# Kernel tuning notes

Measured on AMD Instinct MI355X. Metric: run time of the kernel, lower is better.

The kernel has to match this reference:

```python
import jax, jax.numpy as jnp
import numpy as np

HEADS = 8
DIM_HEAD = 64
EPS = 1e-5  # PyTorch InstanceNorm default eps


def _instance_norm_lastdim(t):
    # PyTorch InstanceNorm1d on (b*h, n, d) with affine=False normalizes over
    # the last (spatial) axis d per (sample, token), biased variance.
    mu = jnp.mean(t, axis=-1, keepdims=True)
    var = jnp.mean(jnp.square(t - mu), axis=-1, keepdims=True)
    return (t - mu) / jnp.sqrt(var + EPS)


def setup_inputs() -> dict:
    key = jax.random.key(0)
    k1, k2, k3, k4, k5 = jax.random.split(key, 5)
    b, n1, n2, dim = 4, 8192, 8192, 256
    inner = HEADS * DIM_HEAD  # 512
    return {
        "x": jax.random.normal(k1, (b, n1, dim), jnp.float32),
        "z": jax.random.normal(k2, (b, n2, dim), jnp.float32),
        "Wq": jax.random.normal(k3, (dim, inner), jnp.float32) * 0.02,
        "Wkv": jax.random.normal(k4, (dim, 2 * inner), jnp.float32) * 0.02,
        "Wout": jax.random.normal(k5, (inner, dim), jnp.float32) * 0.02,
        "bout": jnp.zeros((dim,), jnp.float32),
    }


def reference(x, z, Wq, Wkv, Wout, bout):
    b, n1, _ = x.shape
    n2 = z.shape[1]
    h, d = HEADS, DIM_HEAD

    q = x @ Wq                     # [b, n1, h*d]
    kv = z @ Wkv                   # [b, n2, 2*h*d]
    k, v = jnp.split(kv, 2, axis=-1)

    q = q.reshape(b, n1, h, d).transpose(0, 2, 1, 3)  # b h n1 d
    k = k.reshape(b, n2, h, d).transpose(0, 2, 1, 3)  # b h n2 d
    v = v.reshape(b, n2, h, d).transpose(0, 2, 1, 3)  # b h n2 d

    # galerkin: normalize k and v
    k = _instance_norm_lastdim(k)
    v = _instance_norm_lastdim(v)

    # linear-attention kernel trick: (k^T v) then q @ dots, scaled by 1/n2
    dots = jnp.einsum('bhnd,bhne->bhde', k, v)          # [b, h, d, d]
    out = jnp.einsum('bhnd,bhde->bhne', q, dots) / n2   # [b, h, n1, d]

    out = out.transpose(0, 2, 1, 3).reshape(b, n1, h * d)
    return out @ Wout + bout
```

## Files before the change

kernel.cpp:

```cpp
#include <hip/hip_runtime.h>
#include <cstddef>

#define NB    4
#define NTOK  8192
#define DIMX  256
#define NH    8
#define HD    64
#define INNER 512
#define SPLIT 32
#define EPS   1e-5f

typedef __attribute__((ext_vector_type(8))) short short8;
typedef __attribute__((ext_vector_type(4))) float f32x4;

__device__ __forceinline__ unsigned short f2bf(float f) {
  union { float f; unsigned u; } v; v.f = f;
  unsigned r = v.u + 0x7fffu + ((v.u >> 16) & 1u);
  return (unsigned short)(r >> 16);
}

__global__ __launch_bounds__(256) void k_pre(
    const float* __restrict__ z, unsigned short* __restrict__ zb,
    const float* __restrict__ Wkv, unsigned short* __restrict__ wkvT)
{
  __shared__ unsigned short t[64][68];
  if (blockIdx.x < 2048) {
    const size_t i = ((size_t)blockIdx.x * 256 + threadIdx.x) * 16;
    float4 a0 = *(const float4*)(z + i);
    float4 a1 = *(const float4*)(z + i + 4);
    float4 a2 = *(const float4*)(z + i + 8);
    float4 a3 = *(const float4*)(z + i + 12);
    short8 p0, p1;
    p0[0] = (short)f2bf(a0.x); p0[1] = (short)f2bf(a0.y);
    p0[2] = (short)f2bf(a0.z); p0[3] = (short)f2bf(a0.w);
    p0[4] = (short)f2bf(a1.x); p0[5] = (short)f2bf(a1.y);
    p0[6] = (short)f2bf(a1.z); p0[7] = (short)f2bf(a1.w);
    p1[0] = (short)f2bf(a2.x); p1[1] = (short)f2bf(a2.y);
    p1[2] = (short)f2bf(a2.z); p1[3] = (short)f2bf(a2.w);
    p1[4] = (short)f2bf(a3.x); p1[5] = (short)f2bf(a3.y);
    p1[6] = (short)f2bf(a3.z); p1[7] = (short)f2bf(a3.w);
    *(short8*)(zb + i) = p0;
    *(short8*)(zb + i + 8) = p1;
  } else {
    const int tid = threadIdx.x;
    const int bb = blockIdx.x - 2048;
    const int r0 = (bb & 3) * 64;
    const int c0 = (bb >> 2) * 64;
    const int r = tid >> 2;
    const int c4 = (tid & 3) * 16;
#pragma unroll
    for (int j = 0; j < 4; ++j) {
      float4 v = *(const float4*)(Wkv + (size_t)(r0 + r) * (2 * INNER) + c0 + c4 + j * 4);
      t[r][c4 + j * 4 + 0] = f2bf(v.x);
      t[r][c4 + j * 4 + 1] = f2bf(v.y);
      t[r][c4 + j * 4 + 2] = f2bf(v.z);
      t[r][c4 + j * 4 + 3] = f2bf(v.w);
    }
    __syncthreads();
    const int cc = tid >> 2;
    const int rr4 = (tid & 3) * 16;
    short8 o0, o1;
#pragma unroll
    for (int i = 0; i < 8; ++i) o0[i] = (short)t[rr4 + i][cc];
#pragma unroll
    for (int i = 0; i < 8; ++i) o1[i] = (short)t[rr4 + 8 + i][cc];
    unsigned short* dst = wkvT + (size_t)(c0 + cc) * DIMX + r0 + rr4;
    *(short8*)(dst) = o0;
    *(short8*)(dst + 8) = o1;
  }
}

__global__ __launch_bounds__(256, 2) void k_dots_mfma(
    const unsigned short* __restrict__ zb, const unsigned short* __restrict__ wkvT,
    float* __restrict__ partial)
{
  const int tid  = threadIdx.x;
  const int lane = tid & 63;
  const int w    = tid >> 6;
  const int wm   = w >> 1;
  const int wn   = w & 1;
  const int l15  = lane & 15;
  const int lg   = lane >> 4;

  const int bid = blockIdx.x;
  const int s = bid & (SPLIT - 1);
  const int h = (bid >> 5) & (NH - 1);
  const int b = bid >> 8;

  __shared__ unsigned short zs[2][32][268];
  __shared__ unsigned short kv2[2][128][36];

  short8 awf[4][8];
#pragma unroll
  for (int mf = 0; mf < 4; ++mf) {
    const int dim = wm * 64 + mf * 16 + l15;
    const int gd = (dim < HD) ? (h * HD + dim) : (INNER + h * HD + (dim - HD));
    const unsigned short* base = wkvT + (size_t)gd * DIMX + lg * 8;
#pragma unroll
    for (int kk = 0; kk < 8; ++kk)
      awf[mf][kk] = *(const short8*)(base + kk * 32);
  }

  f32x4 dacc[4];
#pragma unroll
  for (int nf = 0; nf < 4; ++nf) dacc[nf] = (f32x4){0.f, 0.f, 0.f, 0.f};

  const int zr = tid >> 3;
  const int zc = (tid & 7) * 32;
  const unsigned short* zbase = zb + ((size_t)b * NTOK + s * 256 + zr) * DIMX + zc;

  {
    short8 pre[4];
#pragma unroll
    for (int j = 0; j < 4; ++j) pre[j] = *(const short8*)(zbase + j * 8);
#pragma unroll
    for (int j = 0; j < 4; ++j) *(short8*)&zs[0][zr][zc + j * 8] = pre[j];
  }
  __syncthreads();

  int cur = 0;
  for (int tile = 0; tile < 8; ++tile) {
    short8 pre[4];
    if (tile < 7) {
      const unsigned short* src = zbase + (size_t)(tile + 1) * 32 * DIMX;
#pragma unroll
      for (int j = 0; j < 4; ++j) pre[j] = *(const short8*)(src + j * 8);
    }

    f32x4 acc[4];
#pragma unroll
    for (int mf = 0; mf < 4; ++mf) acc[mf] = (f32x4){0.f, 0.f, 0.f, 0.f};

#pragma unroll
    for (int kk = 0; kk < 8; ++kk) {
      short8 bfr = *(const short8*)&zs[cur][wn * 16 + l15][kk * 32 + lg * 8];
#pragma unroll
      for (int mf = 0; mf < 4; ++mf)
        acc[mf] = __builtin_amdgcn_mfma_f32_16x16x32_bf16(
            awf[mf][kk], bfr, acc[mf], 0, 0, 0);
    }

    float a = 0.f, q = 0.f;
#pragma unroll
    for (int mf = 0; mf < 4; ++mf)
#pragma unroll
      for (int r = 0; r < 4; ++r) {
        float v = acc[mf][r];
        a += v; q += v * v;
      }
    a += __shfl_xor(a, 16); a += __shfl_xor(a, 32);
    q += __shfl_xor(q, 16); q += __shfl_xor(q, 32);
    const float mu = a * (1.f / 64.f);
    const float rs = rsqrtf(q * (1.f / 64.f) - mu * mu + EPS);

#pragma unroll
    for (int mf = 0; mf < 4; ++mf)
#pragma unroll
      for (int r = 0; r < 4; ++r)
        kv2[cur][wm * 64 + mf * 16 + lg * 4 + r][wn * 16 + l15] =
            f2bf((acc[mf][r] - mu) * rs);

    if (tile < 7) {
#pragma unroll
      for (int j = 0; j < 4; ++j) *(short8*)&zs[cur ^ 1][zr][zc + j * 8] = pre[j];
    }
    __syncthreads();

    {
      short8 a2 = *(const short8*)&kv2[cur][w * 16 + l15][lg * 8];
#pragma unroll
      for (int nf = 0; nf < 4; ++nf) {
        short8 b2 = *(const short8*)&kv2[cur][64 + nf * 16 + l15][lg * 8];
        dacc[nf] = __builtin_amdgcn_mfma_f32_16x16x32_bf16(a2, b2, dacc[nf], 0, 0, 0);
      }
    }
    cur ^= 1;
  }

  float* pb = partial + ((size_t)((b * NH + h) * SPLIT + s)) * 4096;
#pragma unroll
  for (int nf = 0; nf < 4; ++nf)
#pragma unroll
    for (int r = 0; r < 4; ++r)
      pb[(w * 16 + lg * 4 + r) * 64 + nf * 16 + l15] = dacc[nf][r];
}

__global__ __launch_bounds__(256) void k_reduce(
    const float* __restrict__ partial, float* __restrict__ dots)
{
  const int idx = blockIdx.x * 256 + threadIdx.x;
  const int bh = idx >> 12;
  const int de = idx & 4095;
  const float* p = partial + (size_t)bh * SPLIT * 4096 + de;
  float s = 0.f;
#pragma unroll
  for (int i = 0; i < SPLIT; ++i) s += p[(size_t)i * 4096];
  dots[idx] = s * (1.f / (float)NTOK);
}

__global__ __launch_bounds__(256) void k_bdwout(
    const float* __restrict__ dots, const float* __restrict__ Wout,
    float* __restrict__ tmp)
{
  const int bid = blockIdx.x;
  const int b = bid >> 7;
  const int r4 = (bid & 127) * 4;
  const int h = r4 >> 6;
  const int c = threadIdx.x;
  const float* dr = dots + (size_t)(b * NH + h) * 4096 + (size_t)(r4 & 63) * 64;
  float a0 = 0.f, a1 = 0.f, a2 = 0.f, a3 = 0.f;
#pragma unroll 8
  for (int j = 0; j < 64; ++j) {
    const float wv = Wout[(size_t)(h * 64 + j) * DIMX + c];
    a0 += dr[j] * wv;
    a1 += dr[64 + j] * wv;
    a2 += dr[128 + j] * wv;
    a3 += dr[192 + j] * wv;
  }
  float* tb = tmp + ((size_t)b * INNER + r4) * DIMX + c;
  tb[0] = a0; tb[DIMX] = a1; tb[2 * DIMX] = a2; tb[3 * DIMX] = a3;
}

__global__ __launch_bounds__(256) void k_weff(
    const float* __restrict__ Wq, const float* __restrict__ tmp,
    unsigned short* __restrict__ weffT)
{
  const int bid = blockIdx.x;
  const int b = bid >> 6;
  const int r4 = (bid & 63) * 4;
  const int c = threadIdx.x;
  const float* tb = tmp + (size_t)b * INNER * DIMX + c;
  float a0 = 0.f, a1 = 0.f, a2 = 0.f, a3 = 0.f;
#pragma unroll 8
  for (int k = 0; k < INNER; ++k) {
    const float t = tb[(size_t)k * DIMX];
    a0 += Wq[(size_t)(r4 + 0) * INNER + k] * t;
    a1 += Wq[(size_t)(r4 + 1) * INNER + k] * t;
    a2 += Wq[(size_t)(r4 + 2) * INNER + k] * t;
    a3 += Wq[(size_t)(r4 + 3) * INNER + k] * t;
  }
  unsigned short* wb = weffT + ((size_t)b * DIMX + c) * DIMX + r4;
  wb[0] = f2bf(a0); wb[1] = f2bf(a1); wb[2] = f2bf(a2); wb[3] = f2bf(a3);
}

__global__ __launch_bounds__(256) void k_out_mfma(
    const float* __restrict__ x, const unsigned short* __restrict__ weffT,
    const float* __restrict__ bout, float* __restrict__ out)
{
  const int tid  = threadIdx.x;
  const int lane = tid & 63;
  const int w    = tid >> 6;
  const int l15  = lane & 15;
  const int lg   = lane >> 4;

  const int bid = blockIdx.x;
  const int mt = bid & 127;
  const int b  = bid >> 7;
  const int tok0 = mt * 64;

  __shared__ unsigned short wsl[2][256 * 36];

  short8 afr[8];
  {
    const float* xr = x + ((size_t)b * NTOK + tok0 + w * 16 + l15) * DIMX + lg * 8;
#pragma unroll
    for (int kk = 0; kk < 8; ++kk) {
      float4 xa = *(const float4*)(xr + kk * 32);
      float4 xb = *(const float4*)(xr + kk * 32 + 4);
      short8 a;
      a[0] = (short)f2bf(xa.x); a[1] = (short)f2bf(xa.y);
      a[2] = (short)f2bf(xa.z); a[3] = (short)f2bf(xa.w);
      a[4] = (short)f2bf(xb.x); a[5] = (short)f2bf(xb.y);
      a[6] = (short)f2bf(xb.z); a[7] = (short)f2bf(xb.w);
      afr[kk] = a;
    }
  }

  f32x4 acc[16];
#pragma unroll
  for (int nf = 0; nf < 16; ++nf) acc[nf] = (f32x4){0.f, 0.f, 0.f, 0.f};

  const unsigned short* wb = weffT + (size_t)b * DIMX * DIMX + (size_t)tid * DIMX;

  {
#pragma unroll
    for (int j = 0; j < 4; ++j) {
      short8 g = *(const short8*)(wb + j * 8);
      *(short8*)&wsl[0][tid * 36 + j * 8] = g;
    }
  }
  __syncthreads();

  for (int kk = 0; kk < 8; ++kk) {
    short8 g[4];
    if (kk < 7) {
#pragma unroll
      for (int j = 0; j < 4; ++j)
        g[j] = *(const short8*)(wb + (kk + 1) * 32 + j * 8);
    }
#pragma unroll
    for (int nf = 0; nf < 16; ++nf) {
      short8 b2 = *(const short8*)&wsl[kk & 1][(nf * 16 + l15) * 36 + lg * 8];
      acc[nf] = __builtin_amdgcn_mfma_f32_16x16x32_bf16(afr[kk], b2, acc[nf], 0, 0, 0);
    }
    if (kk < 7) {
#pragma unroll
      for (int j = 0; j < 4; ++j)
        *(short8*)&wsl[(kk + 1) & 1][tid * 36 + j * 8] = g[j];
    }
    __syncthreads();
  }

#pragma unroll
  for (int nf = 0; nf < 16; ++nf) {
    const float bias = bout[nf * 16 + l15];
#pragma unroll
    for (int r = 0; r < 4; ++r) {
      const int row = tok0 + w * 16 + lg * 4 + r;
      out[((size_t)b * NTOK + row) * DIMX + nf * 16 + l15] = acc[nf][r] + bias;
    }
  }
}

extern "C" void kernel_launch(void* const* d_in, const int* in_sizes, int n_in,
                              void* d_out, int out_size, void* d_ws, size_t ws_size,
                              hipStream_t stream) {
  const float* x    = (const float*)d_in[0];
  const float* z    = (const float*)d_in[1];
  const float* Wq   = (const float*)d_in[2];
  const float* Wkv  = (const float*)d_in[3];
  const float* Wout = (const float*)d_in[4];
  const float* bout = (const float*)d_in[5];
  float* out = (float*)d_out;

  float* ws   = (float*)d_ws;
  float* dots = ws;
  float* tmp  = dots + (size_t)NB * NH * 4096;
  unsigned short* wkvT  = (unsigned short*)(tmp + (size_t)NB * INNER * DIMX);
  unsigned short* weffT = wkvT + (size_t)(2 * INNER) * DIMX;

  unsigned short* zbf = (unsigned short*)d_out;
  float* partial = (float*)((char*)d_out + ((size_t)16 << 20));

  k_pre<<<2112, 256, 0, stream>>>(z, zbf, Wkv, wkvT);
  k_dots_mfma<<<NB * NH * SPLIT, 256, 0, stream>>>(zbf, wkvT, partial);
  k_reduce<<<512, 256, 0, stream>>>(partial, dots);
  k_bdwout<<<NB * 128, 256, 0, stream>>>(dots, Wout, tmp);
  k_weff<<<NB * 64, 256, 0, stream>>>(Wq, tmp, weffT);
  k_out_mfma<<<NB * 128, 256, 0, stream>>>(x, weffT, bout, out);
}
```

Measured before the change: 103.3 us.

## Fuse z bf16 conversion into dots kernel and reduction into Wout projection

Removes the separate z fp32→bf16 pre-pass: the dots kernel now loads fp32 z directly and converts while staging into LDS, avoiding a full write and reread of a bf16 copy of z. The split-K partial reduction is folded into the Wout projection kernel, which sums partials into shared memory, eliminating one launch and the dots buffer. The trade-off is that the dots kernel now reads twice the bytes per tile and holds more prefetch registers, and partial rows are reread by several blocks.

```diff
diff --git a/kernel.cpp b/kernel.cpp
--- a/kernel.cpp
+++ b/kernel.cpp
@@ -19,59 +19,47 @@
   return (unsigned short)(r >> 16);
 }
 
-__global__ __launch_bounds__(256) void k_pre(
-    const float* __restrict__ z, unsigned short* __restrict__ zb,
+__device__ __forceinline__ short8 cvt8(float4 a, float4 b) {
+  short8 p;
+  p[0] = (short)f2bf(a.x); p[1] = (short)f2bf(a.y);
+  p[2] = (short)f2bf(a.z); p[3] = (short)f2bf(a.w);
+  p[4] = (short)f2bf(b.x); p[5] = (short)f2bf(b.y);
+  p[6] = (short)f2bf(b.z); p[7] = (short)f2bf(b.w);
+  return p;
+}
+
+__global__ __launch_bounds__(256) void k_wkvT(
     const float* __restrict__ Wkv, unsigned short* __restrict__ wkvT)
 {
   __shared__ unsigned short t[64][68];
-  if (blockIdx.x < 2048) {
-    const size_t i = ((size_t)blockIdx.x * 256 + threadIdx.x) * 16;
-    float4 a0 = *(const float4*)(z + i);
-    float4 a1 = *(const float4*)(z + i + 4);
-    float4 a2 = *(const float4*)(z + i + 8);
-    float4 a3 = *(const float4*)(z + i + 12);
-    short8 p0, p1;
-    p0[0] = (short)f2bf(a0.x); p0[1] = (short)f2bf(a0.y);
-    p0[2] = (short)f2bf(a0.z); p0[3] = (short)f2bf(a0.w);
-    p0[4] = (short)f2bf(a1.x); p0[5] = (short)f2bf(a1.y);
-    p0[6] = (short)f2bf(a1.z); p0[7] = (short)f2bf(a1.w);
-    p1[0] = (short)f2bf(a2.x); p1[1] = (short)f2bf(a2.y);
-    p1[2] = (short)f2bf(a2.z); p1[3] = (short)f2bf(a2.w);
-    p1[4] = (short)f2bf(a3.x); p1[5] = (short)f2bf(a3.y);
-    p1[6] = (short)f2bf(a3.z); p1[7] = (short)f2bf(a3.w);
-    *(short8*)(zb + i) = p0;
-    *(short8*)(zb + i + 8) = p1;
-  } else {
-    const int tid = threadIdx.x;
-    const int bb = blockIdx.x - 2048;
-    const int r0 = (bb & 3) * 64;
-    const int c0 = (bb >> 2) * 64;
-    const int r = tid >> 2;
-    const int c4 = (tid & 3) * 16;
-#pragma unroll
-    for (int j = 0; j < 4; ++j) {
-      float4 v = *(const float4*)(Wkv + (size_t)(r0 + r) * (2 * INNER) + c0 + c4 + j * 4);
-      t[r][c4 + j * 4 + 0] = f2bf(v.x);
-      t[r][c4 + j * 4 + 1] = f2bf(v.y);
-      t[r][c4 + j * 4 + 2] = f2bf(v.z);
-      t[r][c4 + j * 4 + 3] = f2bf(v.w);
-    }
-    __syncthreads();
-    const int cc = tid >> 2;
-    const int rr4 = (tid & 3) * 16;
-    short8 o0, o1;
-#pragma unroll
-    for (int i = 0; i < 8; ++i) o0[i] = (short)t[rr4 + i][cc];
-#pragma unroll
-    for (int i = 0; i < 8; ++i) o1[i] = (short)t[rr4 + 8 + i][cc];
-    unsigned short* dst = wkvT + (size_t)(c0 + cc) * DIMX + r0 + rr4;
-    *(short8*)(dst) = o0;
-    *(short8*)(dst + 8) = o1;
-  }
+  const int tid = threadIdx.x;
+  const int r0 = (blockIdx.x & 3) * 64;
+  const int c0 = (blockIdx.x >> 2) * 64;
+  const int r = tid >> 2;
+  const int c4 = (tid & 3) * 16;
+#pragma unroll
+  for (int j = 0; j < 4; ++j) {
+    float4 v = *(const float4*)(Wkv + (size_t)(r0 + r) * (2 * INNER) + c0 + c4 + j * 4);
+    t[r][c4 + j * 4 + 0] = f2bf(v.x);
+    t[r][c4 + j * 4 + 1] = f2bf(v.y);
+    t[r][c4 + j * 4 + 2] = f2bf(v.z);
+    t[r][c4 + j * 4 + 3] = f2bf(v.w);
+  }
+  __syncthreads();
+  const int cc = tid >> 2;
+  const int rr4 = (tid & 3) * 16;
+  short8 o0, o1;
+#pragma unroll
+  for (int i = 0; i < 8; ++i) o0[i] = (short)t[rr4 + i][cc];
+#pragma unroll
+  for (int i = 0; i < 8; ++i) o1[i] = (short)t[rr4 + 8 + i][cc];
+  unsigned short* dst = wkvT + (size_t)(c0 + cc) * DIMX + r0 + rr4;
+  *(short8*)(dst) = o0;
+  *(short8*)(dst + 8) = o1;
 }
 
 __global__ __launch_bounds__(256, 2) void k_dots_mfma(
-    const unsigned short* __restrict__ zb, const unsigned short* __restrict__ wkvT,
+    const float* __restrict__ z, const unsigned short* __restrict__ wkvT,
     float* __restrict__ partial)
 {
   const int tid  = threadIdx.x;
@@ -107,24 +95,25 @@
 
   const int zr = tid >> 3;
   const int zc = (tid & 7) * 32;
-  const unsigned short* zbase = zb + ((size_t)b * NTOK + s * 256 + zr) * DIMX + zc;
+  const float* zbase = z + ((size_t)b * NTOK + s * 256 + zr) * DIMX + zc;
 
   {
-    short8 pre[4];
-#pragma unroll
-    for (int j = 0; j < 4; ++j) pre[j] = *(const short8*)(zbase + j * 8);
-#pragma unroll
-    for (int j = 0; j < 4; ++j) *(short8*)&zs[0][zr][zc + j * 8] = pre[j];
+    float4 pre[8];
+#pragma unroll
+    for (int j = 0; j < 8; ++j) pre[j] = *(const float4*)(zbase + j * 4);
+#pragma unroll
+    for (int j = 0; j < 4; ++j)
+      *(short8*)&zs[0][zr][zc + j * 8] = cvt8(pre[2 * j], pre[2 * j + 1]);
   }
   __syncthreads();
 
   int cur = 0;
   for (int tile = 0; tile < 8; ++tile) {
-    short8 pre[4];
+    float4 pre[8];
     if (tile < 7) {
-      const unsigned short* src = zbase + (size_t)(tile + 1) * 32 * DIMX;
-#pragma unroll
-      for (int j = 0; j < 4; ++j) pre[j] = *(const short8*)(src + j * 8);
+      const float* src = zbase + (size_t)(tile + 1) * 32 * DIMX;
+#pragma unroll
+      for (int j = 0; j < 8; ++j) pre[j] = *(const float4*)(src + j * 4);
     }
 
     f32x4 acc[4];
@@ -162,7 +151,8 @@
 
     if (tile < 7) {
 #pragma unroll
-      for (int j = 0; j < 4; ++j) *(short8*)&zs[cur ^ 1][zr][zc + j * 8] = pre[j];
+      for (int j = 0; j < 4; ++j)
+        *(short8*)&zs[cur ^ 1][zr][zc + j * 8] = cvt8(pre[2 * j], pre[2 * j + 1]);
     }
     __syncthreads();
 
@@ -185,21 +175,8 @@
       pb[(w * 16 + lg * 4 + r) * 64 + nf * 16 + l15] = dacc[nf][r];
 }
 
-__global__ __launch_bounds__(256) void k_reduce(
-    const float* __restrict__ partial, float* __restrict__ dots)
-{
-  const int idx = blockIdx.x * 256 + threadIdx.x;
-  const int bh = idx >> 12;
-  const int de = idx & 4095;
-  const float* p = partial + (size_t)bh * SPLIT * 4096 + de;
-  float s = 0.f;
-#pragma unroll
-  for (int i = 0; i < SPLIT; ++i) s += p[(size_t)i * 4096];
-  dots[idx] = s * (1.f / (float)NTOK);
-}
-
-__global__ __launch_bounds__(256) void k_bdwout(
-    const float* __restrict__ dots, const float* __restrict__ Wout,
+__global__ __launch_bounds__(256) void k_bdwout2(
+    const float* __restrict__ partial, const float* __restrict__ Wout,
     float* __restrict__ tmp)
 {
   const int bid = blockIdx.x;
@@ -207,15 +184,28 @@
   const int r4 = (bid & 127) * 4;
   const int h = r4 >> 6;
   const int c = threadIdx.x;
-  const float* dr = dots + (size_t)(b * NH + h) * 4096 + (size_t)(r4 & 63) * 64;
+
+  __shared__ float drow[4][64];
+  {
+    const int rr = c >> 6;
+    const int j = c & 63;
+    const float* p = partial + (size_t)(b * NH + h) * SPLIT * 4096
+                   + ((r4 & 63) + rr) * 64 + j;
+    float s = 0.f;
+#pragma unroll
+    for (int i = 0; i < SPLIT; ++i) s += p[(size_t)i * 4096];
+    drow[rr][j] = s * (1.f / (float)NTOK);
+  }
+  __syncthreads();
+
   float a0 = 0.f, a1 = 0.f, a2 = 0.f, a3 = 0.f;
 #pragma unroll 8
   for (int j = 0; j < 64; ++j) {
     const float wv = Wout[(size_t)(h * 64 + j) * DIMX + c];
-    a0 += dr[j] * wv;
-    a1 += dr[64 + j] * wv;
-    a2 += dr[128 + j] * wv;
-    a3 += dr[192 + j] * wv;
+    a0 += drow[0][j] * wv;
+    a1 += drow[1][j] * wv;
+    a2 += drow[2][j] * wv;
+    a3 += drow[3][j] * wv;
   }
   float* tb = tmp + ((size_t)b * INNER + r4) * DIMX + c;
   tb[0] = a0; tb[DIMX] = a1; tb[2 * DIMX] = a2; tb[3 * DIMX] = a3;
@@ -267,12 +257,7 @@
     for (int kk = 0; kk < 8; ++kk) {
       float4 xa = *(const float4*)(xr + kk * 32);
       float4 xb = *(const float4*)(xr + kk * 32 + 4);
-      short8 a;
-      a[0] = (short)f2bf(xa.x); a[1] = (short)f2bf(xa.y);
-      a[2] = (short)f2bf(xa.z); a[3] = (short)f2bf(xa.w);
-      a[4] = (short)f2bf(xb.x); a[5] = (short)f2bf(xb.y);
-      a[6] = (short)f2bf(xb.z); a[7] = (short)f2bf(xb.w);
-      afr[kk] = a;
+      afr[kk] = cvt8(xa, xb);
     }
   }
 
@@ -333,19 +318,16 @@
   const float* bout = (const float*)d_in[5];
   float* out = (float*)d_out;
 
-  float* ws   = (float*)d_ws;
-  float* dots = ws;
-  float* tmp  = dots + (size_t)NB * NH * 4096;
+  float* ws  = (float*)d_ws;
+  float* tmp = ws;
   unsigned short* wkvT  = (unsigned short*)(tmp + (size_t)NB * INNER * DIMX);
   unsigned short* weffT = wkvT + (size_t)(2 * INNER) * DIMX;
 
-  unsigned short* zbf = (unsigned short*)d_out;
-  float* partial = (float*)((char*)d_out + ((size_t)16 << 20));
-
-  k_pre<<<2112, 256, 0, stream>>>(z, zbf, Wkv, wkvT);
-  k_dots_mfma<<<NB * NH * SPLIT, 256, 0, stream>>>(zbf, wkvT, partial);
-  k_reduce<<<512, 256, 0, stream>>>(partial, dots);
-  k_bdwout<<<NB * 128, 256, 0, stream>>>(dots, Wout, tmp);
+  float* partial = (float*)d_out;
+
+  k_wkvT<<<64, 256, 0, stream>>>(Wkv, wkvT);
+  k_dots_mfma<<<NB * NH * SPLIT, 256, 0, stream>>>(z, wkvT, partial);
+  k_bdwout2<<<NB * 128, 256, 0, stream>>>(partial, Wout, tmp);
   k_weff<<<NB * 64, 256, 0, stream>>>(Wq, tmp, weffT);
   k_out_mfma<<<NB * 128, 256, 0, stream>>>(x, weffT, bout, out);
 }
```

After: 118.8 us. 15.0% more time.
